# Optimization experiments

Hardware: AMD Instinct MI355X
Metric: run time of the kernel (lower is better)

Reference implementation:

```python
import jax, jax.numpy as jnp
import numpy as np


def _minplus(x, W):
    # x: [B, in], W: [out, in] -> y[b,i] = min_j (x[b,j] + W[i,j])
    return jnp.min(x[:, None, :] + W[None, :, :], axis=-1)


def _maxbplus(x, W, b):
    # x: [B, in], W: [out, in], b: [out] -> y[b,i] = max_j (x[b,j] + W[i,j]) + b[i]
    return jnp.max(x[:, None, :] + W[None, :, :], axis=-1) + b


def _basic_block(x, w1, w2, b2, sw1=None, sw2=None, sb2=None):
    out = _maxbplus(_minplus(x, w1), w2, b2)
    sc = x if sw1 is None else _maxbplus(_minplus(x, sw1), sw2, sb2)
    return jnp.minimum(out, sc)


def setup_inputs() -> dict:
    key = jax.random.key(0)
    B, IN, OUT = 1024, 256, 512
    ks = jax.random.split(key, 16)
    s = 0.05
    inp = {
        'x': jax.random.normal(ks[0], (B, IN), jnp.float32),
        # layers 1-3: in==out==IN, no block shortcut params
        'l1_w1': jax.random.normal(ks[1], (IN, IN), jnp.float32) * s,
        'l1_w2': jax.random.normal(ks[2], (IN, IN), jnp.float32) * s,
        'l1_b2': jax.random.normal(ks[3], (IN,), jnp.float32) * s,
        'l2_w1': jax.random.normal(ks[4], (IN, IN), jnp.float32) * s,
        'l2_w2': jax.random.normal(ks[5], (IN, IN), jnp.float32) * s,
        'l2_b2': jax.random.normal(ks[6], (IN,), jnp.float32) * s,
        'l3_w1': jax.random.normal(ks[7], (IN, IN), jnp.float32) * s,
        'l3_w2': jax.random.normal(ks[8], (IN, IN), jnp.float32) * s,
        'l3_b2': jax.random.normal(ks[9], (IN,), jnp.float32) * s,
        # layer 4: IN -> OUT, has block-level shortcut
        'l4_w1': jax.random.normal(ks[10], (OUT, IN), jnp.float32) * s,
        'l4_w2': jax.random.normal(ks[11], (OUT, OUT), jnp.float32) * s,
        'l4_b2': jax.random.normal(ks[12], (OUT,), jnp.float32) * s,
        'l4_sw1': jax.random.normal(ks[13], (OUT, IN), jnp.float32) * s,
        'l4_sw2': jax.random.normal(ks[14], (OUT, OUT), jnp.float32) * s,
        'l4_sb2': jax.random.normal(ks[15], (OUT,), jnp.float32) * s,
    }
    k2 = jax.random.split(jax.random.fold_in(key, 1), 3)
    inp['sc_w1'] = jax.random.normal(k2[0], (OUT, IN), jnp.float32) * s
    inp['sc_w2'] = jax.random.normal(k2[1], (OUT, OUT), jnp.float32) * s
    inp['sc_b2'] = jax.random.normal(k2[2], (OUT,), jnp.float32) * s
    return inp


def reference(x, l1_w1, l1_w2, l1_b2, l2_w1, l2_w2, l2_b2,
              l3_w1, l3_w2, l3_b2, l4_w1, l4_w2, l4_b2,
              l4_sw1, l4_sw2, l4_sb2, sc_w1, sc_w2, sc_b2):
    out = _basic_block(x, l1_w1, l1_w2, l1_b2)            # layer1 (IN->IN)
    out = _basic_block(out, l2_w1, l2_w2, l2_b2)          # layer2
    out = _basic_block(out, l3_w1, l3_w2, l3_b2)          # layer3
    out = _basic_block(out, l4_w1, l4_w2, l4_b2,
                       l4_sw1, l4_sw2, l4_sb2)            # layer4 (IN->OUT)
    sc = _maxbplus(_minplus(x, sc_w1), sc_w2, sc_b2)      # bottleneck shortcut
    return jnp.maximum(out, sc)
```

## Files before the change

kernel.cpp:

```cpp
#include <hip/hip_runtime.h>
#include <math.h>


typedef _Float16 h2 __attribute__((ext_vector_type(2)));
typedef _Float16 h8 __attribute__((ext_vector_type(8)));

template<int M> __device__ __forceinline__ h2 rdv(h2 a, h2 b) {
    if constexpr (M) return __builtin_elementwise_max(a, b);
    else             return __builtin_elementwise_min(a, b);
}

struct NetP {
    const float* x;
    const h8 *w11, *w12, *w21, *w22, *w31, *w32;
    const h8 *w41, *w42, *sw1, *sw2, *scw1, *scw2;
    const _Float16 *b12, *b22, *b32, *b42, *sb2, *scb2;
    float* out;
};

template<int ISMAX, int R, int K, bool GOUT>
__device__ __forceinline__ void stage(
    const h8* __restrict__ Wc,
    const _Float16* __restrict__ bias,
    const _Float16* __restrict__ X,
    const _Float16* __restrict__ E1,
    const _Float16* __restrict__ E2,
    _Float16* __restrict__ Y,
    float* __restrict__ gout, int b0,
    h2* __restrict__ part)
{
    constexpr int NRG = R / 2;
    constexpr int KS  = 1024 / NRG;
    static_assert(NRG * KS == 1024, "thread mapping");
    const int tid  = threadIdx.x;
    const int rowg = tid & (NRG - 1);
    const int kq   = tid / NRG;
    const int r0 = rowg, r1 = rowg + NRG;
    constexpr int NC = (K / KS) / 8;
    const int kc0 = kq * NC;

    const h2* Xh2 = (const h2*)X;

    h2 a00, a01, a10, a11;
    {
        h8 w0 = Wc[(size_t)kc0 * R + r0];
        h8 w1 = Wc[(size_t)kc0 * R + r1];
        const h2* xk = Xh2 + kc0 * 16;
        h2 xs0 = xk[0], xs1 = xk[1];
        h2 u = {w0[0], w0[0]}, v = {w1[0], w1[0]};
        a00 = xs0 + u; a01 = xs1 + u;
        a10 = xs0 + v; a11 = xs1 + v;
#pragma unroll
        for (int j = 1; j < 8; ++j) {
            xs0 = xk[2 * j]; xs1 = xk[2 * j + 1];
            h2 uu = {w0[j], w0[j]}, vv = {w1[j], w1[j]};
            a00 = rdv<ISMAX>(a00, xs0 + uu); a01 = rdv<ISMAX>(a01, xs1 + uu);
            a10 = rdv<ISMAX>(a10, xs0 + vv); a11 = rdv<ISMAX>(a11, xs1 + vv);
        }
    }
#pragma unroll 2
    for (int kc = kc0 + 1; kc < kc0 + NC; ++kc) {
        h8 w0 = Wc[(size_t)kc * R + r0];
        h8 w1 = Wc[(size_t)kc * R + r1];
        const h2* xk = Xh2 + kc * 16;
#pragma unroll
        for (int j = 0; j < 8; ++j) {
            h2 xs0 = xk[2 * j], xs1 = xk[2 * j + 1];
            h2 uu = {w0[j], w0[j]}, vv = {w1[j], w1[j]};
            a00 = rdv<ISMAX>(a00, xs0 + uu); a01 = rdv<ISMAX>(a01, xs1 + uu);
            a10 = rdv<ISMAX>(a10, xs0 + vv); a11 = rdv<ISMAX>(a11, xs1 + vv);
        }
    }

    if (kq) {
        h2* pp = part + (size_t)(kq - 1) * R * 2;
        pp[r0 * 2] = a00; pp[r0 * 2 + 1] = a01;
        pp[r1 * 2] = a10; pp[r1 * 2 + 1] = a11;
    }
    __syncthreads();
    if (kq == 0) {
#pragma unroll
        for (int qq = 0; qq < KS - 1; ++qq) {
            const h2* pp = part + (size_t)qq * R * 2;
            a00 = rdv<ISMAX>(a00, pp[r0 * 2]); a01 = rdv<ISMAX>(a01, pp[r0 * 2 + 1]);
            a10 = rdv<ISMAX>(a10, pp[r1 * 2]); a11 = rdv<ISMAX>(a11, pp[r1 * 2 + 1]);
        }
        if (ISMAX) {
            _Float16 q0 = bias[r0], q1 = bias[r1];
            h2 s0 = {q0, q0}, s1 = {q1, q1};
            a00 += s0; a01 += s0; a10 += s1; a11 += s1;
        }
        if (E1) {
            const h2* e = (const h2*)E1;
            a00 = __builtin_elementwise_min(a00, e[r0 * 2]);
            a01 = __builtin_elementwise_min(a01, e[r0 * 2 + 1]);
            a10 = __builtin_elementwise_min(a10, e[r1 * 2]);
            a11 = __builtin_elementwise_min(a11, e[r1 * 2 + 1]);
        }
        if (E2) {
            const h2* e = (const h2*)E2;
            a00 = __builtin_elementwise_max(a00, e[r0 * 2]);
            a01 = __builtin_elementwise_max(a01, e[r0 * 2 + 1]);
            a10 = __builtin_elementwise_max(a10, e[r1 * 2]);
            a11 = __builtin_elementwise_max(a11, e[r1 * 2 + 1]);
        }
        if constexpr (GOUT) {
            gout[(size_t)(b0 + 0) * 512 + r0] = (float)a00[0];
            gout[(size_t)(b0 + 1) * 512 + r0] = (float)a00[1];
            gout[(size_t)(b0 + 2) * 512 + r0] = (float)a01[0];
            gout[(size_t)(b0 + 3) * 512 + r0] = (float)a01[1];
            gout[(size_t)(b0 + 0) * 512 + r1] = (float)a10[0];
            gout[(size_t)(b0 + 1) * 512 + r1] = (float)a10[1];
            gout[(size_t)(b0 + 2) * 512 + r1] = (float)a11[0];
            gout[(size_t)(b0 + 3) * 512 + r1] = (float)a11[1];
        } else {
            h2* y = (h2*)Y;
            y[r0 * 2] = a00; y[r0 * 2 + 1] = a01;
            y[r1 * 2] = a10; y[r1 * 2 + 1] = a11;
        }
    }
    __syncthreads();
}

__global__ __launch_bounds__(1024) void netf(NetP p)
{
    __shared__ __align__(16) _Float16 X0[256 * 4];
    __shared__ __align__(16) _Float16 B0[512 * 4], B1[512 * 4];
    __shared__ __align__(16) _Float16 B2[512 * 4], B3[512 * 4];
    __shared__ __align__(16) h2 part[3584];
    const int tid = threadIdx.x;
    const int b0  = blockIdx.x * 4;

    {
        const int bl = tid >> 8;
        const int k  = tid & 255;
        X0[k * 4 + bl] = (_Float16)p.x[(size_t)(b0 + bl) * 256 + k];
    }
    __syncthreads();

    float* o = p.out;
    stage<0,512,256,false>(p.scw1, nullptr, X0, nullptr, nullptr, B0, o, b0, part);
    stage<1,512,512,false>(p.scw2, p.scb2,  B0, nullptr, nullptr, B1, o, b0, part);
    stage<0,256,256,false>(p.w11, nullptr, X0, nullptr, nullptr, B0, o, b0, part);
    stage<1,256,256,false>(p.w12, p.b12,   B0, X0,      nullptr, B2, o, b0, part);
    stage<0,256,256,false>(p.w21, nullptr, B2, nullptr, nullptr, B0, o, b0, part);
    stage<1,256,256,false>(p.w22, p.b22,   B0, B2,      nullptr, B3, o, b0, part);
    stage<0,256,256,false>(p.w31, nullptr, B3, nullptr, nullptr, B0, o, b0, part);
    stage<1,256,256,false>(p.w32, p.b32,   B0, B3,      nullptr, B2, o, b0, part);
    stage<0,512,256,false>(p.w41, nullptr, B2, nullptr, nullptr, B0, o, b0, part);
    stage<0,512,256,false>(p.sw1, nullptr, B2, nullptr, nullptr, B3, o, b0, part);
    stage<1,512,512,false>(p.w42, p.b42,   B0, nullptr, nullptr, B2, o, b0, part);
    stage<1,512,512,true >(p.sw2, p.sb2,   B3, B2,      B1, nullptr, o, b0, part);
}

struct Prep {
    const float* s[12]; h8* d[12]; int R[12]; int K[12];
    const float* bs[6]; _Float16* bd[6]; int bn[6];
};
__global__ __launch_bounds__(256) void cvtw(Prep p)
{
    const int m = blockIdx.y;
    if (m == 12) {
        if (blockIdx.x != 0) return;
        for (int s = 0; s < 6; ++s)
            for (int i = threadIdx.x; i < p.bn[s]; i += 256)
                p.bd[s][i] = (_Float16)p.bs[s][i];
        return;
    }
    const int R = p.R[m], K = p.K[m];
    const int tilesR = R >> 6;
    const int nt = tilesR * (K >> 6);
    const int t = blockIdx.x;
    if (t >= nt) return;
    const int tr = t % tilesR, tk = t / tilesR;

    __shared__ float s[64][65];
    const int lane = threadIdx.x & 63, ty = threadIdx.x >> 6;
    const float* src = p.s[m];
#pragma unroll
    for (int r = ty; r < 64; r += 4)
        s[r][lane] = src[(size_t)(tr * 64 + r) * K + tk * 64 + lane];
    __syncthreads();
    h8* dst = p.d[m];
#pragma unroll
    for (int c = 0; c < 2; ++c) {
        int cc = ty + c * 4;
        h8 v;
#pragma unroll
        for (int j = 0; j < 8; ++j) v[j] = (_Float16)s[lane][cc * 8 + j];
        dst[(size_t)(tk * 8 + cc) * R + tr * 64 + lane] = v;
    }
}

extern "C" void kernel_launch(void* const* d_in, const int* in_sizes, int n_in,
                              void* d_out, int out_size, void* d_ws, size_t ws_size,
                              hipStream_t stream) {
    (void)in_sizes; (void)n_in; (void)ws_size; (void)out_size;
    const float* fin[19];
    for (int i = 0; i < 19; ++i) fin[i] = (const float*)d_in[i];

    _Float16* hw = (_Float16*)d_ws;

    _Float16* w11c  = hw;
    _Float16* w12c  = hw + 65536;
    _Float16* w21c  = hw + 131072;
    _Float16* w22c  = hw + 196608;
    _Float16* w31c  = hw + 262144;
    _Float16* w32c  = hw + 327680;
    _Float16* w41c  = hw + 393216;
    _Float16* w42c  = hw + 524288;
    _Float16* sw1c  = hw + 786432;
    _Float16* sw2c  = hw + 917504;
    _Float16* scw1c = hw + 1179648;
    _Float16* scw2c = hw + 1310720;
    _Float16* bia   = hw + 1572864;
    _Float16* b12 = bia, *b22 = bia + 256, *b32 = bia + 512;
    _Float16* b42 = bia + 768, *sb2 = bia + 1280, *scb2 = bia + 1792;

    Prep cw;
    const float* wsrc[12] = {fin[1], fin[2], fin[4], fin[5], fin[7], fin[8],
                             fin[10], fin[11], fin[13], fin[14], fin[16], fin[17]};
    _Float16* wdst[12]    = {w11c, w12c, w21c, w22c, w31c, w32c,
                             w41c, w42c, sw1c, sw2c, scw1c, scw2c};
    const int wR[12] = {256,256,256,256,256,256, 512,512,512,512,512,512};
    const int wK[12] = {256,256,256,256,256,256, 256,512,256,512,256,512};
    for (int i = 0; i < 12; ++i) {
        cw.s[i] = wsrc[i]; cw.d[i] = (h8*)wdst[i]; cw.R[i] = wR[i]; cw.K[i] = wK[i];
    }
    const float* bsrc[6] = {fin[3], fin[6], fin[9], fin[12], fin[15], fin[18]};
    _Float16* bdst[6]    = {b12, b22, b32, b42, sb2, scb2};
    const int bn[6]      = {256, 256, 256, 512, 512, 512};
    for (int i = 0; i < 6; ++i) { cw.bs[i] = bsrc[i]; cw.bd[i] = bdst[i]; cw.bn[i] = bn[i]; }

    NetP p;
    p.x   = fin[0];
    p.w11 = (const h8*)w11c; p.w12 = (const h8*)w12c;
    p.w21 = (const h8*)w21c; p.w22 = (const h8*)w22c;
    p.w31 = (const h8*)w31c; p.w32 = (const h8*)w32c;
    p.w41 = (const h8*)w41c; p.w42 = (const h8*)w42c;
    p.sw1 = (const h8*)sw1c; p.sw2 = (const h8*)sw2c;
    p.scw1 = (const h8*)scw1c; p.scw2 = (const h8*)scw2c;
    p.b12 = b12; p.b22 = b22; p.b32 = b32; p.b42 = b42; p.sb2 = sb2; p.scb2 = scb2;
    p.out = (float*)d_out;

    cvtw<<<dim3(64, 13), 256, 0, stream>>>(cw);
    netf<<<dim3(256), dim3(1024), 0, stream>>>(p);
}
```

Before: 80.05 us.

## Process two batch rows per block instead of four, doubling grid size

Each block now handles two batch rows rather than four, so the grid grows from 256 to 512 blocks, and each thread keeps two packed-half accumulators instead of four. The aim is to fill more of the GPU's compute units and shorten each block's critical path of twelve serial stages. The cost is that every weight element fetched is reused across only two batch rows, which doubles total weight traffic from L2/global memory, and the number of block-level barriers executed overall also doubles.

```diff
diff --git a/kernel.cpp b/kernel.cpp
--- a/kernel.cpp
+++ b/kernel.cpp
@@ -36,87 +36,76 @@
     const int rowg = tid & (NRG - 1);
     const int kq   = tid / NRG;
     const int r0 = rowg, r1 = rowg + NRG;
-    constexpr int NC = (K / KS) / 8;
+    constexpr int NC = (K / 8) / KS;
     const int kc0 = kq * NC;
 
     const h2* Xh2 = (const h2*)X;
 
-    h2 a00, a01, a10, a11;
+    h2 a0, a1;
     {
         h8 w0 = Wc[(size_t)kc0 * R + r0];
         h8 w1 = Wc[(size_t)kc0 * R + r1];
-        const h2* xk = Xh2 + kc0 * 16;
-        h2 xs0 = xk[0], xs1 = xk[1];
+        const h2* xk = Xh2 + kc0 * 8;
+        h2 xs = xk[0];
         h2 u = {w0[0], w0[0]}, v = {w1[0], w1[0]};
-        a00 = xs0 + u; a01 = xs1 + u;
-        a10 = xs0 + v; a11 = xs1 + v;
+        a0 = xs + u; a1 = xs + v;
 #pragma unroll
         for (int j = 1; j < 8; ++j) {
-            xs0 = xk[2 * j]; xs1 = xk[2 * j + 1];
+            xs = xk[j];
             h2 uu = {w0[j], w0[j]}, vv = {w1[j], w1[j]};
-            a00 = rdv<ISMAX>(a00, xs0 + uu); a01 = rdv<ISMAX>(a01, xs1 + uu);
-            a10 = rdv<ISMAX>(a10, xs0 + vv); a11 = rdv<ISMAX>(a11, xs1 + vv);
+            a0 = rdv<ISMAX>(a0, xs + uu);
+            a1 = rdv<ISMAX>(a1, xs + vv);
         }
     }
 #pragma unroll 2
     for (int kc = kc0 + 1; kc < kc0 + NC; ++kc) {
         h8 w0 = Wc[(size_t)kc * R + r0];
         h8 w1 = Wc[(size_t)kc * R + r1];
-        const h2* xk = Xh2 + kc * 16;
+        const h2* xk = Xh2 + kc * 8;
 #pragma unroll
         for (int j = 0; j < 8; ++j) {
-            h2 xs0 = xk[2 * j], xs1 = xk[2 * j + 1];
+            h2 xs = xk[j];
             h2 uu = {w0[j], w0[j]}, vv = {w1[j], w1[j]};
-            a00 = rdv<ISMAX>(a00, xs0 + uu); a01 = rdv<ISMAX>(a01, xs1 + uu);
-            a10 = rdv<ISMAX>(a10, xs0 + vv); a11 = rdv<ISMAX>(a11, xs1 + vv);
+            a0 = rdv<ISMAX>(a0, xs + uu);
+            a1 = rdv<ISMAX>(a1, xs + vv);
         }
     }
 
     if (kq) {
-        h2* pp = part + (size_t)(kq - 1) * R * 2;
-        pp[r0 * 2] = a00; pp[r0 * 2 + 1] = a01;
-        pp[r1 * 2] = a10; pp[r1 * 2 + 1] = a11;
+        h2* pp = part + (size_t)(kq - 1) * R;
+        pp[r0] = a0; pp[r1] = a1;
     }
     __syncthreads();
     if (kq == 0) {
 #pragma unroll
         for (int qq = 0; qq < KS - 1; ++qq) {
-            const h2* pp = part + (size_t)qq * R * 2;
-            a00 = rdv<ISMAX>(a00, pp[r0 * 2]); a01 = rdv<ISMAX>(a01, pp[r0 * 2 + 1]);
-            a10 = rdv<ISMAX>(a10, pp[r1 * 2]); a11 = rdv<ISMAX>(a11, pp[r1 * 2 + 1]);
+            const h2* pp = part + (size_t)qq * R;
+            a0 = rdv<ISMAX>(a0, pp[r0]);
+            a1 = rdv<ISMAX>(a1, pp[r1]);
         }
         if (ISMAX) {
             _Float16 q0 = bias[r0], q1 = bias[r1];
             h2 s0 = {q0, q0}, s1 = {q1, q1};
-            a00 += s0; a01 += s0; a10 += s1; a11 += s1;
+            a0 += s0; a1 += s1;
         }
         if (E1) {
             const h2* e = (const h2*)E1;
-            a00 = __builtin_elementwise_min(a00, e[r0 * 2]);
-            a01 = __builtin_elementwise_min(a01, e[r0 * 2 + 1]);
-            a10 = __builtin_elementwise_min(a10, e[r1 * 2]);
-            a11 = __builtin_elementwise_min(a11, e[r1 * 2 + 1]);
+            a0 = __builtin_elementwise_min(a0, e[r0]);
+            a1 = __builtin_elementwise_min(a1, e[r1]);
         }
         if (E2) {
             const h2* e = (const h2*)E2;
-            a00 = __builtin_elementwise_max(a00, e[r0 * 2]);
-            a01 = __builtin_elementwise_max(a01, e[r0 * 2 + 1]);
-            a10 = __builtin_elementwise_max(a10, e[r1 * 2]);
-            a11 = __builtin_elementwise_max(a11, e[r1 * 2 + 1]);
+            a0 = __builtin_elementwise_max(a0, e[r0]);
+            a1 = __builtin_elementwise_max(a1, e[r1]);
         }
         if constexpr (GOUT) {
-            gout[(size_t)(b0 + 0) * 512 + r0] = (float)a00[0];
-            gout[(size_t)(b0 + 1) * 512 + r0] = (float)a00[1];
-            gout[(size_t)(b0 + 2) * 512 + r0] = (float)a01[0];
-            gout[(size_t)(b0 + 3) * 512 + r0] = (float)a01[1];
-            gout[(size_t)(b0 + 0) * 512 + r1] = (float)a10[0];
-            gout[(size_t)(b0 + 1) * 512 + r1] = (float)a10[1];
-            gout[(size_t)(b0 + 2) * 512 + r1] = (float)a11[0];
-            gout[(size_t)(b0 + 3) * 512 + r1] = (float)a11[1];
+            gout[(size_t)(b0 + 0) * 512 + r0] = (float)a0[0];
+            gout[(size_t)(b0 + 1) * 512 + r0] = (float)a0[1];
+            gout[(size_t)(b0 + 0) * 512 + r1] = (float)a1[0];
+            gout[(size_t)(b0 + 1) * 512 + r1] = (float)a1[1];
         } else {
             h2* y = (h2*)Y;
-            y[r0 * 2] = a00; y[r0 * 2 + 1] = a01;
-            y[r1 * 2] = a10; y[r1 * 2 + 1] = a11;
+            y[r0] = a0; y[r1] = a1;
         }
     }
     __syncthreads();
@@ -124,17 +113,17 @@
 
 __global__ __launch_bounds__(1024) void netf(NetP p)
 {
-    __shared__ __align__(16) _Float16 X0[256 * 4];
-    __shared__ __align__(16) _Float16 B0[512 * 4], B1[512 * 4];
-    __shared__ __align__(16) _Float16 B2[512 * 4], B3[512 * 4];
-    __shared__ __align__(16) h2 part[3584];
+    __shared__ __align__(16) _Float16 X0[256 * 2];
+    __shared__ __align__(16) _Float16 B0[512 * 2], B1[512 * 2];
+    __shared__ __align__(16) _Float16 B2[512 * 2], B3[512 * 2];
+    __shared__ __align__(16) h2 part[1792];
     const int tid = threadIdx.x;
-    const int b0  = blockIdx.x * 4;
-
-    {
+    const int b0  = blockIdx.x * 2;
+
+    if (tid < 512) {
         const int bl = tid >> 8;
         const int k  = tid & 255;
-        X0[k * 4 + bl] = (_Float16)p.x[(size_t)(b0 + bl) * 256 + k];
+        X0[k * 2 + bl] = (_Float16)p.x[(size_t)(b0 + bl) * 256 + k];
     }
     __syncthreads();
 
@@ -244,5 +233,5 @@
     p.out = (float*)d_out;
 
     cvtw<<<dim3(64, 13), 256, 0, stream>>>(cw);
-    netf<<<dim3(256), dim3(1024), 0, stream>>>(p);
-}
+    netf<<<dim3(512), dim3(1024), 0, stream>>>(p);
+}
```

After: 78.63 us. About the same (-1.8%).
